# Kernel optimization log

Measured on AMD Instinct MI355X. Metric: run time of the kernel, lower is better.

Reference implementation:

```python
import jax, jax.numpy as jnp
import numpy as np

# Model constants (match init_kwargs / torchcde conventions)
B = 1024        # batch
L = 128         # number of spline knots (grid_points = 0..L-1)
C_IN = 8        # input_channels
HID = 64        # hidden_channels
MLP_H = 128     # CDEFunc hidden width
INIT_H = 20     # initial-network hidden width


def setup_inputs() -> dict:
    key = jax.random.key(0)
    ks = jax.random.split(key, 9)
    # cubic spline coeffs: (B, L-1, 4*C_IN) laid out as [a, b, c, d] per interval
    coeffs = jax.random.normal(ks[0], (B, L - 1, 4 * C_IN), dtype=jnp.float32) * 0.1
    # initial network: C_IN -> 20 -> HID (ReLU, then Tanh)
    Wi1 = jax.random.normal(ks[1], (C_IN, INIT_H), dtype=jnp.float32) / np.sqrt(C_IN)
    bi1 = jnp.zeros((INIT_H,), jnp.float32)
    Wi2 = jax.random.normal(ks[2], (INIT_H, HID), dtype=jnp.float32) / np.sqrt(INIT_H)
    bi2 = jnp.zeros((HID,), jnp.float32)
    # CDE vector field: (HID+1) -> 128 -> C_IN*HID (ReLU, then Tanh)
    W1 = jax.random.normal(ks[3], (HID + 1, MLP_H), dtype=jnp.float32) / np.sqrt(HID + 1)
    b1 = jnp.zeros((MLP_H,), jnp.float32)
    W2 = jax.random.normal(ks[4], (MLP_H, C_IN * HID), dtype=jnp.float32) / np.sqrt(MLP_H)
    b2 = jnp.zeros((C_IN * HID,), jnp.float32)
    return {"coeffs": coeffs, "Wi1": Wi1, "bi1": bi1, "Wi2": Wi2, "bi2": bi2,
            "W1": W1, "b1": b1, "W2": W2, "b2": b2}


def reference(coeffs, Wi1, bi1, Wi2, bi2, W1, b1, W2, b2):
    Lm1 = coeffs.shape[1]
    # a,b,c,d: each (B, L-1, C_IN). X(t) = a + b*f + c*f^2 + d*f^3 on interval idx,
    # dX/dt = b + 2c*f + 3d*f^2, with f = t - idx (torchcde CubicSpline convention).
    a, b, c, d = jnp.split(coeffs, 4, axis=-1)

    def dXdt(t):
        idx = jnp.clip(jnp.floor(t).astype(jnp.int32), 0, Lm1 - 1)
        fr = t - idx
        return b[:, idx] + 2.0 * c[:, idx] * fr + 3.0 * d[:, idx] * fr * fr  # (B, C_IN)

    def cde_func(t, z):
        # FFN([HID+1, 128, C_IN*HID], ReLU hidden, Tanh output) on concat(t, z)
        tz = jnp.concatenate([jnp.full((z.shape[0], 1), t, z.dtype), z], axis=1)
        h = jax.nn.relu(tz @ W1 + b1)
        return jnp.tanh(h @ W2 + b2).reshape(z.shape[0], HID, C_IN)  # (B, HID, C_IN)

    def vf(t, z):
        # dz/dt = f(t,z) @ dX/dt
        return jnp.einsum('bhc,bc->bh', cde_func(t, z), dXdt(t))

    # z0 = initial(X(t0)); X(0) = a at interval 0 with frac 0
    X0 = a[:, 0]
    z0 = jnp.tanh(jax.nn.relu(X0 @ Wi1 + bi1) @ Wi2 + bi2)  # (B, HID)

    def rk4_step(z, i):
        t = i.astype(z.dtype)
        k1 = vf(t, z)
        k2 = vf(t + 0.5, z + 0.5 * k1)
        k3 = vf(t + 0.5, z + 0.5 * k2)
        k4 = vf(t + 1.0, z + k3)
        z_new = z + (k1 + 2.0 * k2 + 2.0 * k3 + k4) / 6.0
        return z_new, z_new

    _, zs = jax.lax.scan(rk4_step, z0, jnp.arange(Lm1))  # (L-1, B, HID)
    # z evaluated at all grid points, like cdeint(t=X.grid_points): (B, L, HID)
    return jnp.concatenate([z0[None], zs], axis=0).transpose(1, 0, 2)
```

## Files before the change

### kernel.cpp

```cpp
#include <hip/hip_runtime.h>
#include <stdint.h>

#define LM1  127
#define NTHR 1024

typedef _Float16 half8_t __attribute__((ext_vector_type(8)));
typedef float    f32x4   __attribute__((ext_vector_type(4)));
typedef float    f32x2   __attribute__((ext_vector_type(2)));

__device__ __forceinline__ float fast_tanh(float x) {
  float e = __expf(2.0f * x);
  return 1.0f - 2.0f * __builtin_amdgcn_rcpf(e + 1.0f);
}

__global__ void __launch_bounds__(NTHR, 4) cde_kernel(
    const float* __restrict__ coeffs,
    const float* __restrict__ Wi1, const float* __restrict__ bi1,
    const float* __restrict__ Wi2, const float* __restrict__ bi2,
    const float* __restrict__ W1,  const float* __restrict__ b1,
    const float* __restrict__ W2,  const float* __restrict__ b2,
    float* __restrict__ out)
{
  __shared__ _Float16 zsb[1024];
  __shared__ _Float16 hA [2048];
  __shared__ float    fwb[16][144];
  __shared__ float    gds[2][3][4][8];

  const int t    = threadIdx.x;
  const int lane = t & 63;
  const int w    = t >> 6;
  const int l15  = lane & 15;
  const int lq   = lane >> 4;
  const int r    = lane & 3;
  const int row0 = blockIdx.x * 4;

  for (int u = t; u < 512;  u += NTHR) ((uint32_t*)zsb)[u] = 0u;
  for (int u = t; u < 1024; u += NTHR) ((uint32_t*)hA)[u]  = 0u;

  half8_t bB[2] = {};
  float w1t_c = 0.f, b1_c = 0.f;
  if (w < 8) {
    #pragma unroll
    for (int kt = 0; kt < 2; ++kt)
      #pragma unroll
      for (int j = 0; j < 8; ++j)
        bB[kt][j] = (_Float16)W1[(1 + kt * 32 + lq * 8 + j) * 128 + w * 16 + l15];
    w1t_c = W1[w * 16 + l15];
    b1_c  = b1[w * 16 + l15];
  }

  half8_t bf[2][4];
  #pragma unroll
  for (int nt = 0; nt < 2; ++nt)
    #pragma unroll
    for (int kt = 0; kt < 4; ++kt)
      #pragma unroll
      for (int j = 0; j < 8; ++j)
        bf[nt][kt][j] =
            (_Float16)W2[(kt * 32 + lq * 8 + j) * 512 + w * 32 + nt * 16 + l15];

  const int q    = lane >> 4;
  const int hxlk = (lane >> 2) & 3;
  const int hxk  = w * 4 + hxlk;
  const float b2r0 = b2[hxk * 8 + 2 * q];
  const float b2r1 = b2[hxk * 8 + 2 * q + 1];

  const int hx = w * 4 + (lane >> 2);
  _Float16* zwp;
  {
    const int kh = hx >> 5, lqw = (hx >> 3) & 3, j = hx & 7;
    zwp = &zsb[8 * (kh * 64 + lqw * 16 + r) + j];
  }
  _Float16* hwp;
  {
    const int col = 16 * w + l15;
    const int ktw = (col >> 5) & 3, lqw2 = (col >> 3) & 3, j2 = col & 7;
    hwp = &hA[8 * (ktw * 64 + lqw2 * 16) + j2];
  }
  float* const fsp = &fwb[w][36 * (l15 >> 3) + 4 * (l15 & 7)];
  const float* const frp = &fwb[w][36 * hxlk + 8 * q + r];

  float z = 0.0f;
  if (lane < 16) {
    const float* cb = coeffs + (size_t)(row0 + r) * (LM1 * 32);
    float x0[8];
    #pragma unroll
    for (int c = 0; c < 8; ++c) x0[c] = cb[c];
    float acc = bi2[hx];
    for (int j = 0; j < 20; ++j) {
      float u = bi1[j];
      #pragma unroll
      for (int c = 0; c < 8; ++c) u += x0[c] * Wi1[c * 20 + j];
      acc += fmaxf(u, 0.0f) * Wi2[j * 64 + hx];
    }
    z = fast_tanh(acc);
    out[(size_t)(row0 + r) * 8192 + hx] = z;
  }

  const int rg = (t >> 3) & 3, cg = t & 7;
  const float* cbp = coeffs + (size_t)(row0 + rg) * (LM1 * 32);
  float pb = 0.f, pc = 0.f, pd = 0.f, pbn = 0.f;
  if (t < 32) { pb = cbp[8 + cg]; pc = cbp[16 + cg]; pd = cbp[24 + cg]; pbn = cbp[40 + cg]; }

  __syncthreads();

  for (int i = 0; i < LM1; ++i) {
    if (t < 32) {
      gds[i & 1][0][rg][cg] = pb;
      gds[i & 1][1][rg][cg] = pb + pc + 0.75f * pd;
      gds[i & 1][2][rg][cg] = (i < LM1 - 1) ? pbn : fmaf(3.0f, pd, fmaf(2.0f, pc, pb));
      if (i + 1 < LM1) {
        const float* nb = cbp + (size_t)(i + 1) * 32;
        pb = nb[8 + cg]; pc = nb[16 + cg]; pd = nb[24 + cg];
        pbn = (i + 2 < LM1) ? nb[40 + cg] : 0.0f;
      }
    }

    float ksum = 0.0f, kprev = 0.0f;
    #pragma unroll
    for (int s = 0; s < 4; ++s) {
      const float coef = (s == 0) ? 0.0f : (s == 3) ? 1.0f : 0.5f;
      const float ts   = (float)i + ((s == 0) ? 0.0f : (s == 3) ? 1.0f : 0.5f);
      const int   gi   = (s == 0) ? 0 : (s == 3) ? 2 : 1;

      if (lane < 16) *zwp = (_Float16)(z + coef * kprev);
      __syncthreads();

      if (w < 8) {
        const half8_t a0 = *(const half8_t*)(zsb + 8 * lane);
        const half8_t a1 = *(const half8_t*)(zsb + 512 + 8 * lane);
        f32x4 hd = {0.f, 0.f, 0.f, 0.f};
        hd = __builtin_amdgcn_mfma_f32_16x16x32_f16(a0, bB[0], hd, 0, 0, 0);
        hd = __builtin_amdgcn_mfma_f32_16x16x32_f16(a1, bB[1], hd, 0, 0, 0);
        if (lane < 16) {
          const float hb = fmaf(ts, w1t_c, b1_c);
          hwp[0]  = (_Float16)fmaxf(hd.x + hb, 0.0f);
          hwp[8]  = (_Float16)fmaxf(hd.y + hb, 0.0f);
          hwp[16] = (_Float16)fmaxf(hd.z + hb, 0.0f);
          hwp[24] = (_Float16)fmaxf(hd.w + hb, 0.0f);
        }
      }
      __syncthreads();

      {
        half8_t ha[4];
        #pragma unroll
        for (int kt = 0; kt < 4; ++kt)
          ha[kt] = *(const half8_t*)(hA + 512 * kt + 8 * lane);
        f32x4 d0 = {0.f, 0.f, 0.f, 0.f}, d1 = d0;
        #pragma unroll
        for (int kt = 0; kt < 4; ++kt) {
          d0 = __builtin_amdgcn_mfma_f32_16x16x32_f16(ha[kt], bf[0][kt], d0, 0, 0, 0);
          d1 = __builtin_amdgcn_mfma_f32_16x16x32_f16(ha[kt], bf[1][kt], d1, 0, 0, 0);
        }
        if (lane < 16) {
          *(f32x4*)(fsp)      = d0;
          *(f32x4*)(fsp + 72) = d1;
        }
      }
      asm volatile("s_waitcnt lgkmcnt(0)" ::: "memory");

      {
        const float v0 = frp[0], v1 = frp[4];
        const f32x2 gv = *(const f32x2*)&gds[i & 1][gi][r][2 * q];
        float kcv = fast_tanh(v0 + b2r0) * gv.x + fast_tanh(v1 + b2r1) * gv.y;
        kcv += __shfl_xor(kcv, 16, 64);
        kcv += __shfl_xor(kcv, 32, 64);
        kprev = kcv;
        ksum += ((s == 1 || s == 2) ? 2.0f : 1.0f) * kcv;
      }
    }
    if (lane < 16) {
      z += ksum * (1.0f / 6.0f);
      out[(size_t)(row0 + r) * 8192 + (size_t)(i + 1) * 64 + hx] = z;
    }
  }
}

extern "C" void kernel_launch(void* const* d_in, const int* in_sizes, int n_in,
                              void* d_out, int out_size, void* d_ws, size_t ws_size,
                              hipStream_t stream) {
  const float* coeffs = (const float*)d_in[0];
  const float* Wi1    = (const float*)d_in[1];
  const float* bi1    = (const float*)d_in[2];
  const float* Wi2    = (const float*)d_in[3];
  const float* bi2    = (const float*)d_in[4];
  const float* W1     = (const float*)d_in[5];
  const float* b1     = (const float*)d_in[6];
  const float* W2     = (const float*)d_in[7];
  const float* b2     = (const float*)d_in[8];
  float* out          = (float*)d_out;
  (void)in_sizes; (void)n_in; (void)out_size; (void)d_ws; (void)ws_size;
  cde_kernel<<<256, NTHR, 0, stream>>>(coeffs, Wi1, bi1, Wi2, bi2,
                                       W1, b1, W2, b2, out);
}
```

Baseline: 537.6 us.

## Load spline coefficients per lane in registers and compact padded MFMA LDS buffers

Each lane now loads its own two spline-derivative coefficients straight from global memory into registers and prefetches two intervals ahead. This removes the shared-memory staging array gds and the 32-thread producer path. The LDS buffers for z and the hidden activations shrink to only the four live rows, and MFMA A-operands are zero-filled in registers for the padding rows, so the zero-initialisation loops go away. The cost is more redundant global loads per block, since many lanes read the same coefficients, plus extra register pressure.

```diff
diff --git a/kernel.cpp b/kernel.cpp
--- a/kernel.cpp
+++ b/kernel.cpp
@@ -6,7 +6,6 @@
 
 typedef _Float16 half8_t __attribute__((ext_vector_type(8)));
 typedef float    f32x4   __attribute__((ext_vector_type(4)));
-typedef float    f32x2   __attribute__((ext_vector_type(2)));
 
 __device__ __forceinline__ float fast_tanh(float x) {
   float e = __expf(2.0f * x);
@@ -21,10 +20,9 @@
     const float* __restrict__ W2,  const float* __restrict__ b2,
     float* __restrict__ out)
 {
-  __shared__ _Float16 zsb[1024];
-  __shared__ _Float16 hA [2048];
+  __shared__ _Float16 zsb[256];
+  __shared__ _Float16 hA [512];
   __shared__ float    fwb[16][144];
-  __shared__ float    gds[2][3][4][8];
 
   const int t    = threadIdx.x;
   const int lane = t & 63;
@@ -33,9 +31,6 @@
   const int lq   = lane >> 4;
   const int r    = lane & 3;
   const int row0 = blockIdx.x * 4;
-
-  for (int u = t; u < 512;  u += NTHR) ((uint32_t*)zsb)[u] = 0u;
-  for (int u = t; u < 1024; u += NTHR) ((uint32_t*)hA)[u]  = 0u;
 
   half8_t bB[2] = {};
   float w1t_c = 0.f, b1_c = 0.f;
@@ -60,25 +55,20 @@
             (_Float16)W2[(kt * 32 + lq * 8 + j) * 512 + w * 32 + nt * 16 + l15];
 
   const int q    = lane >> 4;
-  const int hxlk = (lane >> 2) & 3;
-  const int hxk  = w * 4 + hxlk;
+  const int hxl  = (lane >> 2) & 3;
+  const int hxk  = w * 4 + hxl;
   const float b2r0 = b2[hxk * 8 + 2 * q];
   const float b2r1 = b2[hxk * 8 + 2 * q + 1];
 
-  const int hx = w * 4 + (lane >> 2);
-  _Float16* zwp;
-  {
-    const int kh = hx >> 5, lqw = (hx >> 3) & 3, j = hx & 7;
-    zwp = &zsb[8 * (kh * 64 + lqw * 16 + r) + j];
-  }
+  const int hxo = w * 4 + (lane >> 2);
+  _Float16* const zwp = &zsb[(hxo >> 5) * 128 + ((hxo >> 3) & 3) * 32 + r * 8 + (hxo & 7)];
   _Float16* hwp;
   {
     const int col = 16 * w + l15;
-    const int ktw = (col >> 5) & 3, lqw2 = (col >> 3) & 3, j2 = col & 7;
-    hwp = &hA[8 * (ktw * 64 + lqw2 * 16) + j2];
+    hwp = &hA[((col >> 5) & 3) * 128 + ((col >> 3) & 3) * 32 + (col & 7)];
   }
   float* const fsp = &fwb[w][36 * (l15 >> 3) + 4 * (l15 & 7)];
-  const float* const frp = &fwb[w][36 * hxlk + 8 * q + r];
+  const float* const frp = &fwb[w][36 * hxl + 8 * q + r];
 
   float z = 0.0f;
   if (lane < 16) {
@@ -86,34 +76,39 @@
     float x0[8];
     #pragma unroll
     for (int c = 0; c < 8; ++c) x0[c] = cb[c];
-    float acc = bi2[hx];
+    float acc = bi2[hxo];
     for (int j = 0; j < 20; ++j) {
       float u = bi1[j];
       #pragma unroll
       for (int c = 0; c < 8; ++c) u += x0[c] * Wi1[c * 20 + j];
-      acc += fmaxf(u, 0.0f) * Wi2[j * 64 + hx];
+      acc += fmaxf(u, 0.0f) * Wi2[j * 64 + hxo];
     }
     z = fast_tanh(acc);
-    out[(size_t)(row0 + r) * 8192 + hx] = z;
+    out[(size_t)(row0 + r) * 8192 + hxo] = z;
   }
 
-  const int rg = (t >> 3) & 3, cg = t & 7;
-  const float* cbp = coeffs + (size_t)(row0 + rg) * (LM1 * 32);
-  float pb = 0.f, pc = 0.f, pd = 0.f, pbn = 0.f;
-  if (t < 32) { pb = cbp[8 + cg]; pc = cbp[16 + cg]; pd = cbp[24 + cg]; pbn = cbp[40 + cg]; }
+  const float* const gbase = coeffs + (size_t)(row0 + r) * (LM1 * 32);
+  const int c0 = 2 * q, c1 = 2 * q + 1;
+  float cb0 = gbase[8 + c0],  cc0 = gbase[16 + c0],  cd0 = gbase[24 + c0];
+  float cb1 = gbase[8 + c1],  cc1 = gbase[16 + c1],  cd1 = gbase[24 + c1];
+  float nb0 = gbase[32 + 8 + c0], nc0 = gbase[32 + 16 + c0], nd0 = gbase[32 + 24 + c0];
+  float nb1 = gbase[32 + 8 + c1], nc1 = gbase[32 + 16 + c1], nd1 = gbase[32 + 24 + c1];
 
   __syncthreads();
 
   for (int i = 0; i < LM1; ++i) {
-    if (t < 32) {
-      gds[i & 1][0][rg][cg] = pb;
-      gds[i & 1][1][rg][cg] = pb + pc + 0.75f * pd;
-      gds[i & 1][2][rg][cg] = (i < LM1 - 1) ? pbn : fmaf(3.0f, pd, fmaf(2.0f, pc, pb));
-      if (i + 1 < LM1) {
-        const float* nb = cbp + (size_t)(i + 1) * 32;
-        pb = nb[8 + cg]; pc = nb[16 + cg]; pd = nb[24 + cg];
-        pbn = (i + 2 < LM1) ? nb[40 + cg] : 0.0f;
-      }
+    float g0_[3], g1_[3];
+    g0_[0] = cb0; g0_[1] = cb0 + cc0 + 0.75f * cd0;
+    g0_[2] = (i < LM1 - 1) ? nb0 : fmaf(3.0f, cd0, fmaf(2.0f, cc0, cb0));
+    g1_[0] = cb1; g1_[1] = cb1 + cc1 + 0.75f * cd1;
+    g1_[2] = (i < LM1 - 1) ? nb1 : fmaf(3.0f, cd1, fmaf(2.0f, cc1, cb1));
+    cb0 = nb0; cc0 = nc0; cd0 = nd0;
+    cb1 = nb1; cc1 = nc1; cd1 = nd1;
+    {
+      const int i2 = (i + 2 < LM1) ? (i + 2) : (LM1 - 1);
+      const float* nb = gbase + (size_t)i2 * 32;
+      nb0 = nb[8 + c0]; nc0 = nb[16 + c0]; nd0 = nb[24 + c0];
+      nb1 = nb[8 + c1]; nc1 = nb[16 + c1]; nd1 = nb[24 + c1];
     }
 
     float ksum = 0.0f, kprev = 0.0f;
@@ -127,8 +122,11 @@
       __syncthreads();
 
       if (w < 8) {
-        const half8_t a0 = *(const half8_t*)(zsb + 8 * lane);
-        const half8_t a1 = *(const half8_t*)(zsb + 512 + 8 * lane);
+        half8_t a0 = {}, a1 = {};
+        if (l15 < 4) {
+          a0 = *(const half8_t*)(zsb + 8 * (4 * lq + l15));
+          a1 = *(const half8_t*)(zsb + 128 + 8 * (4 * lq + l15));
+        }
         f32x4 hd = {0.f, 0.f, 0.f, 0.f};
         hd = __builtin_amdgcn_mfma_f32_16x16x32_f16(a0, bB[0], hd, 0, 0, 0);
         hd = __builtin_amdgcn_mfma_f32_16x16x32_f16(a1, bB[1], hd, 0, 0, 0);
@@ -143,10 +141,12 @@
       __syncthreads();
 
       {
-        half8_t ha[4];
-        #pragma unroll
-        for (int kt = 0; kt < 4; ++kt)
-          ha[kt] = *(const half8_t*)(hA + 512 * kt + 8 * lane);
+        half8_t ha[4] = {{}, {}, {}, {}};
+        if (l15 < 4) {
+          #pragma unroll
+          for (int kt = 0; kt < 4; ++kt)
+            ha[kt] = *(const half8_t*)(hA + kt * 128 + lq * 32 + l15 * 8);
+        }
         f32x4 d0 = {0.f, 0.f, 0.f, 0.f}, d1 = d0;
         #pragma unroll
         for (int kt = 0; kt < 4; ++kt) {
@@ -162,8 +162,7 @@
 
       {
         const float v0 = frp[0], v1 = frp[4];
-        const f32x2 gv = *(const f32x2*)&gds[i & 1][gi][r][2 * q];
-        float kcv = fast_tanh(v0 + b2r0) * gv.x + fast_tanh(v1 + b2r1) * gv.y;
+        float kcv = fast_tanh(v0 + b2r0) * g0_[gi] + fast_tanh(v1 + b2r1) * g1_[gi];
         kcv += __shfl_xor(kcv, 16, 64);
         kcv += __shfl_xor(kcv, 32, 64);
         kprev = kcv;
@@ -172,7 +171,7 @@
     }
     if (lane < 16) {
       z += ksum * (1.0f / 6.0f);
-      out[(size_t)(row0 + r) * 8192 + (size_t)(i + 1) * 64 + hx] = z;
+      out[(size_t)(row0 + r) * 8192 + (size_t)(i + 1) * 64 + hxo] = z;
     }
   }
 }
```

New measurement: 675.9 us. 25.7% more time.
